# Optimization experiments

Measured on AMD Instinct MI355X. Metric: run time of the kernel, lower is better.

The kernel has to match this reference:

```python
import jax, jax.numpy as jnp
import numpy as np

DIM_Q = 512
DIM_KV = 512
HEADS = 8
EPS = 1e-5


def _layernorm(x, gamma, beta):
    mu = jnp.mean(x, axis=-1, keepdims=True)
    var = jnp.var(x, axis=-1, keepdims=True)
    return (x - mu) * jax.lax.rsqrt(var + EPS) * gamma + beta


def setup_inputs() -> dict:
    key = jax.random.key(0)
    ks = jax.random.split(key, 12)
    B, N, M = 4, 2048, 2048
    s_q = 1.0 / np.sqrt(DIM_Q)
    s_kv = 1.0 / np.sqrt(DIM_KV)
    return {
        "x": jax.random.normal(ks[0], (B, N, DIM_Q), jnp.float32),
        "context": jax.random.normal(ks[1], (B, M, DIM_KV), jnp.float32),
        "g_q": jnp.ones((DIM_Q,), jnp.float32),
        "b_q": jnp.zeros((DIM_Q,), jnp.float32),
        "g_kv": jnp.ones((DIM_KV,), jnp.float32),
        "b_kv": jnp.zeros((DIM_KV,), jnp.float32),
        "Wq": jax.random.uniform(ks[2], (DIM_Q, DIM_Q), jnp.float32, -s_q, s_q),
        "bq": jax.random.uniform(ks[3], (DIM_Q,), jnp.float32, -s_q, s_q),
        "Wk": jax.random.uniform(ks[4], (DIM_KV, DIM_Q), jnp.float32, -s_kv, s_kv),
        "bk": jax.random.uniform(ks[5], (DIM_Q,), jnp.float32, -s_kv, s_kv),
        "Wv": jax.random.uniform(ks[6], (DIM_KV, DIM_Q), jnp.float32, -s_kv, s_kv),
        "bv": jax.random.uniform(ks[7], (DIM_Q,), jnp.float32, -s_kv, s_kv),
        "Wo": jax.random.uniform(ks[8], (DIM_Q, DIM_Q), jnp.float32, -s_q, s_q),
        "bo": jax.random.uniform(ks[9], (DIM_Q,), jnp.float32, -s_q, s_q),
    }


def reference(x, context, g_q, b_q, g_kv, b_kv, Wq, bq, Wk, bk, Wv, bv, Wo, bo):
    B, N, C = x.shape
    M = context.shape[1]
    H = HEADS
    D = C // H
    scale = D ** (-0.5)

    residual = x
    xn = _layernorm(x, g_q, b_q)
    cn = _layernorm(context, g_kv, b_kv)

    # projections: [B, S, C] -> [B, H, S, D]
    q = (xn @ Wq + bq).reshape(B, N, H, D).transpose(0, 2, 1, 3)
    k = (cn @ Wk + bk).reshape(B, M, H, D).transpose(0, 2, 1, 3)
    v = (cn @ Wv + bv).reshape(B, M, H, D).transpose(0, 2, 1, 3)

    attn = jax.nn.softmax(jnp.einsum('bhnd,bhmd->bhnm', q, k) * scale, axis=-1)
    out = jnp.einsum('bhnm,bhmd->bhnd', attn, v)
    out = out.transpose(0, 2, 1, 3).reshape(B, N, C)
    # dropout is identity in eval mode
    return residual + out @ Wo + bo
```

## Files before the change

### kernel.cpp

```cpp
#include <hip/hip_runtime.h>
#include <hip/hip_bf16.h>

#define DIMC 512
#define NB   2048
#define MB   2048
#define ROWS 8192

typedef __attribute__((ext_vector_type(8))) short s8v;
typedef __attribute__((ext_vector_type(4))) short s4v;
typedef __attribute__((ext_vector_type(4))) float f4v;

__device__ __forceinline__ unsigned short cvt_bf16(float x) {
  union { float f; unsigned u; } v; v.f = x;
  unsigned r = v.u + 0x7fffu + ((v.u >> 16) & 1u);
  return (unsigned short)(r >> 16);
}

__device__ __forceinline__ void gload16(const void* g, void* l) {
  __builtin_amdgcn_global_load_lds(
      (const __attribute__((address_space(1))) unsigned int*)g,
      (__attribute__((address_space(3))) unsigned int*)l, 16, 0, 0);
}

__device__ __forceinline__ unsigned cvt_pk_bf16(float a, float b) {
  unsigned r;
  asm("v_cvt_pk_bf16_f32 %0, %1, %2" : "=v"(r) : "v"(a), "v"(b));
  return r;
}

__global__ void ln_kernel(const float* __restrict__ x, const float* __restrict__ ctx,
                          const float* __restrict__ gq, const float* __restrict__ bq,
                          const float* __restrict__ gkv, const float* __restrict__ bkv,
                          unsigned short* __restrict__ xn, unsigned short* __restrict__ cn) {
  int row  = blockIdx.x * 4 + (threadIdx.x >> 6);
  int lane = threadIdx.x & 63;
  const float* src; unsigned short* dst; const float* g; const float* b;
  if (row < ROWS) { src = x   + (size_t)row * DIMC;        dst = xn + (size_t)row * DIMC;        g = gq;  b = bq;  }
  else            { src = ctx + (size_t)(row-ROWS) * DIMC; dst = cn + (size_t)(row-ROWS) * DIMC; g = gkv; b = bkv; }

  float4 v0 = ((const float4*)src)[lane];
  float4 v1 = ((const float4*)src)[lane + 64];
  float s  = v0.x+v0.y+v0.z+v0.w + v1.x+v1.y+v1.z+v1.w;
  float ss = v0.x*v0.x+v0.y*v0.y+v0.z*v0.z+v0.w*v0.w
           + v1.x*v1.x+v1.y*v1.y+v1.z*v1.z+v1.w*v1.w;
  #pragma unroll
  for (int m = 1; m <= 32; m <<= 1) { s += __shfl_xor(s, m); ss += __shfl_xor(ss, m); }
  float mu  = s * (1.0f/512.0f);
  float var = ss * (1.0f/512.0f) - mu*mu;
  float rs  = rsqrtf(var + 1e-5f);

  int i0 = lane*4, i1 = 256 + lane*4;
  ushort4 o0, o1;
  o0.x = cvt_bf16((v0.x-mu)*rs*g[i0+0] + b[i0+0]);
  o0.y = cvt_bf16((v0.y-mu)*rs*g[i0+1] + b[i0+1]);
  o0.z = cvt_bf16((v0.z-mu)*rs*g[i0+2] + b[i0+2]);
  o0.w = cvt_bf16((v0.w-mu)*rs*g[i0+3] + b[i0+3]);
  o1.x = cvt_bf16((v1.x-mu)*rs*g[i1+0] + b[i1+0]);
  o1.y = cvt_bf16((v1.y-mu)*rs*g[i1+1] + b[i1+1]);
  o1.z = cvt_bf16((v1.z-mu)*rs*g[i1+2] + b[i1+2]);
  o1.w = cvt_bf16((v1.w-mu)*rs*g[i1+3] + b[i1+3]);
  *(ushort4*)&dst[i0] = o0;
  *(ushort4*)&dst[i1] = o1;
}

__global__ void wt_kernel(const float* __restrict__ Wq, const float* __restrict__ Wk,
                          const float* __restrict__ Wv, const float* __restrict__ Wo,
                          unsigned short* __restrict__ Wt) {
  __shared__ float tile[64][65];
  int z = blockIdx.z;
  const float* W = (z==0) ? Wq : (z==1) ? Wk : (z==2) ? Wv : Wo;
  unsigned short* dst = Wt + (size_t)z * DIMC * DIMC;
  int k0 = blockIdx.x * 64, n0 = blockIdx.y * 64;
  int tid = threadIdx.x;
  #pragma unroll
  for (int i = 0; i < 16; ++i) {
    int idx = tid + i*256; int r = idx >> 6, c = idx & 63;
    tile[r][c] = W[(size_t)(k0+r)*DIMC + n0 + c];
  }
  __syncthreads();
  #pragma unroll
  for (int i = 0; i < 16; ++i) {
    int idx = tid + i*256; int r = idx >> 6, c = idx & 63;
    dst[(size_t)(n0+r)*DIMC + k0 + c] = cvt_bf16(tile[c][r]);
  }
}

__global__ void gemm_qkv(const unsigned short* __restrict__ xn, const unsigned short* __restrict__ cnr,
                         const unsigned short* __restrict__ Wt,
                         const float* __restrict__ bq, const float* __restrict__ bk, const float* __restrict__ bv,
                         unsigned short* __restrict__ Qo, unsigned short* __restrict__ Ko,
                         unsigned short* __restrict__ Vo) {
  int z = blockIdx.z;
  const unsigned short* A = (z == 0) ? xn : cnr;
  const unsigned short* B = Wt + (size_t)z * DIMC * DIMC;
  const float* bias       = (z==0) ? bq : (z==1) ? bk : bv;
  unsigned short* C       = (z==0) ? Qo : (z==1) ? Ko : Vo;
  const float cs          = (z==0) ? 0.18033688011f : 1.0f;

  __shared__ unsigned short As[128][64];
  __shared__ unsigned short Bs[128][64];

  int tid = threadIdx.x;
  int w = tid >> 6, lane = tid & 63;
  int wr = w >> 1, wc = w & 1;
  int mBase = blockIdx.x * 128, nBase = blockIdx.y * 128;

  f4v zf = {0.f, 0.f, 0.f, 0.f};
  f4v acc[4][4];
  #pragma unroll
  for (int m = 0; m < 4; ++m)
    #pragma unroll
    for (int n = 0; n < 4; ++n) acc[m][n] = zf;

  const unsigned short* gA = A + (size_t)(mBase + (lane>>3)) * DIMC + (lane&7)*8;
  const unsigned short* gB = B + (size_t)(nBase + (lane>>3)) * DIMC + (lane&7)*8;

  for (int kt = 0; kt < 8; ++kt) {
    int k0 = kt * 64;
    if (kt) __syncthreads();
    #pragma unroll
    for (int r = 0; r < 4; ++r) {
      int row0 = r*32 + w*8;
      gload16(gA + (size_t)row0 * DIMC + k0, &As[row0][0]);
      gload16(gB + (size_t)row0 * DIMC + k0, &Bs[row0][0]);
    }
    __syncthreads();
    #pragma unroll
    for (int t = 0; t < 2; ++t) {
      s8v af[4], bfr[4];
      #pragma unroll
      for (int m = 0; m < 4; ++m)
        af[m] = *(const s8v*)&As[wr*64 + m*16 + (lane&15)][t*32 + (lane>>4)*8];
      #pragma unroll
      for (int n = 0; n < 4; ++n)
        bfr[n] = *(const s8v*)&Bs[wc*64 + n*16 + (lane&15)][t*32 + (lane>>4)*8];
      #pragma unroll
      for (int m = 0; m < 4; ++m)
        #pragma unroll
        for (int n = 0; n < 4; ++n)
          acc[m][n] = __builtin_amdgcn_mfma_f32_16x16x32_bf16(af[m], bfr[n], acc[m][n], 0, 0, 0);
    }
  }

  if (z == 2) {
    #pragma unroll
    for (int m = 0; m < 4; ++m) {
      int row = mBase + wr*64 + m*16 + (lane>>4)*4;
      int b_  = row >> 11, key = row & 2047;
      int k   = key >> 2;
      int P0  = (((k>>2)&1)<<2) + ((k&3)<<3) + ((k>>3)<<5);
      #pragma unroll
      for (int n = 0; n < 4; ++n) {
        int col = nBase + wc*64 + n*16 + (lane&15);
        float bb = bias[col];
        ushort4 st;
        st.x = cvt_bf16(acc[m][n][0] + bb);
        st.y = cvt_bf16(acc[m][n][1] + bb);
        st.z = cvt_bf16(acc[m][n][2] + bb);
        st.w = cvt_bf16(acc[m][n][3] + bb);
        *(ushort4*)&C[((size_t)(b_*8 + (col>>6))*64 + (col&63))*2048 + P0] = st;
      }
    }
  } else {
    #pragma unroll
    for (int m = 0; m < 4; ++m) {
      int row = mBase + wr*64 + m*16 + (lane>>4)*4;
      #pragma unroll
      for (int n = 0; n < 4; ++n) {
        int col = nBase + wc*64 + n*16 + (lane&15);
        float bb = bias[col];
        #pragma unroll
        for (int j = 0; j < 4; ++j)
          C[(size_t)(row+j)*DIMC + col] = cvt_bf16((acc[m][n][j] + bb) * cs);
      }
    }
  }
}

__global__ void gemm_out(const unsigned short* __restrict__ A, const unsigned short* __restrict__ Bt,
                         const float* __restrict__ bo, const float* __restrict__ resid,
                         float* __restrict__ out) {
  __shared__ unsigned short As[128][64];
  __shared__ unsigned short Bs[128][64];

  int tid = threadIdx.x;
  int w = tid >> 6, lane = tid & 63;
  int wr = w >> 1, wc = w & 1;
  int mBase = blockIdx.x * 128, nBase = blockIdx.y * 128;

  f4v zf = {0.f, 0.f, 0.f, 0.f};
  f4v acc[4][4];
  #pragma unroll
  for (int m = 0; m < 4; ++m)
    #pragma unroll
    for (int n = 0; n < 4; ++n) acc[m][n] = zf;

  const unsigned short* gA = A  + (size_t)(mBase + (lane>>3)) * DIMC + (lane&7)*8;
  const unsigned short* gB = Bt + (size_t)(nBase + (lane>>3)) * DIMC + (lane&7)*8;

  for (int kt = 0; kt < 8; ++kt) {
    int k0 = kt * 64;
    if (kt) __syncthreads();
    #pragma unroll
    for (int r = 0; r < 4; ++r) {
      int row0 = r*32 + w*8;
      gload16(gA + (size_t)row0 * DIMC + k0, &As[row0][0]);
      gload16(gB + (size_t)row0 * DIMC + k0, &Bs[row0][0]);
    }
    __syncthreads();
    #pragma unroll
    for (int t = 0; t < 2; ++t) {
      s8v af[4], bfr[4];
      #pragma unroll
      for (int m = 0; m < 4; ++m)
        af[m] = *(const s8v*)&As[wr*64 + m*16 + (lane&15)][t*32 + (lane>>4)*8];
      #pragma unroll
      for (int n = 0; n < 4; ++n)
        bfr[n] = *(const s8v*)&Bs[wc*64 + n*16 + (lane&15)][t*32 + (lane>>4)*8];
      #pragma unroll
      for (int m = 0; m < 4; ++m)
        #pragma unroll
        for (int n = 0; n < 4; ++n)
          acc[m][n] = __builtin_amdgcn_mfma_f32_16x16x32_bf16(af[m], bfr[n], acc[m][n], 0, 0, 0);
    }
  }

  #pragma unroll
  for (int m = 0; m < 4; ++m) {
    int row = mBase + wr*64 + m*16 + (lane>>4)*4;
    #pragma unroll
    for (int n = 0; n < 4; ++n) {
      int col = nBase + wc*64 + n*16 + (lane&15);
      float bb = bo[col];
      #pragma unroll
      for (int j = 0; j < 4; ++j) {
        size_t idx = (size_t)(row+j)*DIMC + col;
        out[idx] = acc[m][n][j] + bb + resid[idx];
      }
    }
  }
}

__global__ void attn_kernel(const unsigned short* __restrict__ Q, const unsigned short* __restrict__ K,
                            const unsigned short* __restrict__ Vt, unsigned short* __restrict__ O) {
  __shared__ __align__(16) char Ks[2][8192];
  __shared__ __align__(16) char Vs[2][8192];

  int tid = threadIdx.x, w = tid >> 6, lane = tid & 63;
  int slot = blockIdx.x;
  int logical = (slot & 7) * 128 + (slot >> 3);
  int qb = logical & 31;
  int bh = logical >> 5;
  int b = bh >> 3, h = bh & 7;
  size_t base  = ((size_t)b * NB) * DIMC + h * 64;
  size_t vbase = (size_t)(b*8 + h) * 64 * 2048;

  int g = lane >> 4;
  int l15 = lane & 15;

  int qrow = qb*64 + w*16 + l15;
  const s8v qf0 = *(const s8v*)&Q[base + (size_t)qrow*DIMC + g*8];
  const s8v qf1 = *(const s8v*)&Q[base + (size_t)qrow*DIMC + 32 + g*8];

  f4v zf = {0.f, 0.f, 0.f, 0.f};
  f4v o_[4];
  #pragma unroll
  for (int c = 0; c < 4; ++c) o_[c] = zf;
  f4v o5 = zf;

  s8v ones;
  #pragma unroll
  for (int e = 0; e < 8; ++e) ones[e] = (short)0x3F80;

  int sub = lane >> 3;
  int grp = ((lane & 7) ^ sub) * 8;
  const unsigned short* Kg = K + base;
  const unsigned short* Vg = Vt + vbase;
  int krow0 = w*16 + sub,  krow1 = w*16 + 8 + sub;
  unsigned sdst0 = (unsigned)(w*2048);
  unsigned sdst1 = (unsigned)(w*2048 + 1024);

  int sw = (l15 & 7) << 4;
  unsigned a0 = (unsigned)(l15*128 + ((16*g) ^ sw));
  unsigned a1 = (unsigned)(l15*128 + (((64 + 16*g)) ^ sw));

  gload16(Kg + (size_t)(krow0)*DIMC + grp, Ks[0] + sdst0);
  gload16(Kg + (size_t)(krow1)*DIMC + grp, Ks[0] + sdst1);
  gload16(Vg + (size_t)(krow0)*2048 + grp, Vs[0] + sdst0);
  gload16(Vg + (size_t)(krow1)*2048 + grp, Vs[0] + sdst1);

  #pragma unroll 1
  for (int tt = 0; tt < 16; ++tt) {
    #pragma unroll
    for (int p = 0; p < 2; ++p) {
      int t = tt*2 + p;
      const char* KsB = Ks[p];
      const char* VsB = Vs[p];
      char* KsN = Ks[p^1];
      char* VsN = Vs[p^1];

      if (t < 31) {
        int kv = (t+1)*64;
        gload16(Kg + (size_t)(kv + krow0)*DIMC + grp, KsN + sdst0);
        gload16(Kg + (size_t)(kv + krow1)*DIMC + grp, KsN + sdst1);
        gload16(Vg + (size_t)(krow0)*2048 + kv + grp, VsN + sdst0);
        gload16(Vg + (size_t)(krow1)*2048 + kv + grp, VsN + sdst1);
        asm volatile("s_waitcnt vmcnt(4)" ::: "memory");
      } else {
        asm volatile("s_waitcnt vmcnt(0)" ::: "memory");
      }
      __builtin_amdgcn_s_barrier();
      __builtin_amdgcn_sched_barrier(0);

      f4v st[4];
      #pragma unroll
      for (int c = 0; c < 4; ++c) {
        s8v ka = *(const s8v*)(KsB + c*2048 + a0);
        s8v kb = *(const s8v*)(KsB + c*2048 + a1);
        st[c] = __builtin_amdgcn_mfma_f32_16x16x32_bf16(ka, qf0, zf, 0, 0, 0);
        st[c] = __builtin_amdgcn_mfma_f32_16x16x32_bf16(kb, qf1, st[c], 0, 0, 0);
      }

      s8v vf0[4], vf1[4];
      #pragma unroll
      for (int c = 0; c < 4; ++c) {
        vf0[c] = *(const s8v*)(VsB + c*2048 + a0);
        vf1[c] = *(const s8v*)(VsB + c*2048 + a1);
      }

      float pt[4][4];
      #pragma unroll
      for (int c = 0; c < 4; ++c)
        #pragma unroll
        for (int j = 0; j < 4; ++j)
          pt[c][j] = __builtin_amdgcn_exp2f(st[c][j]);

      union { unsigned i[8]; s8v s[2]; } pu;
      pu.i[0] = cvt_pk_bf16(pt[0][0], pt[0][1]);
      pu.i[1] = cvt_pk_bf16(pt[0][2], pt[0][3]);
      pu.i[2] = cvt_pk_bf16(pt[1][0], pt[1][1]);
      pu.i[3] = cvt_pk_bf16(pt[1][2], pt[1][3]);
      pu.i[4] = cvt_pk_bf16(pt[2][0], pt[2][1]);
      pu.i[5] = cvt_pk_bf16(pt[2][2], pt[2][3]);
      pu.i[6] = cvt_pk_bf16(pt[3][0], pt[3][1]);
      pu.i[7] = cvt_pk_bf16(pt[3][2], pt[3][3]);

      #pragma unroll
      for (int c = 0; c < 4; ++c) {
        o_[c] = __builtin_amdgcn_mfma_f32_16x16x32_bf16(pu.s[0], vf0[c], o_[c], 0, 0, 0);
        o_[c] = __builtin_amdgcn_mfma_f32_16x16x32_bf16(pu.s[1], vf1[c], o_[c], 0, 0, 0);
      }
      o5 = __builtin_amdgcn_mfma_f32_16x16x32_bf16(pu.s[0], ones, o5, 0, 0, 0);
      o5 = __builtin_amdgcn_mfma_f32_16x16x32_bf16(pu.s[1], ones, o5, 0, 0, 0);

      __builtin_amdgcn_sched_barrier(0);
      __builtin_amdgcn_s_barrier();
    }
  }

  float lb[4];
  #pragma unroll
  for (int j = 0; j < 4; ++j) lb[j] = 1.0f / o5[j];
  int nrow = qb*64 + w*16 + g*4;
  #pragma unroll
  for (int c = 0; c < 4; ++c) {
    int d = h*64 + c*16 + l15;
    #pragma unroll
    for (int j = 0; j < 4; ++j)
      O[((size_t)b*NB + nrow + j) * DIMC + d] = cvt_bf16(o_[c][j] * lb[j]);
  }
}

extern "C" void kernel_launch(void* const* d_in, const int* in_sizes, int n_in,
                              void* d_out, int out_size, void* d_ws, size_t ws_size,
                              hipStream_t stream) {
  const float* x    = (const float*)d_in[0];
  const float* ctx  = (const float*)d_in[1];
  const float* g_q  = (const float*)d_in[2];
  const float* b_q  = (const float*)d_in[3];
  const float* g_kv = (const float*)d_in[4];
  const float* b_kv = (const float*)d_in[5];
  const float* Wq   = (const float*)d_in[6];
  const float* bq   = (const float*)d_in[7];
  const float* Wk   = (const float*)d_in[8];
  const float* bk   = (const float*)d_in[9];
  const float* Wv   = (const float*)d_in[10];
  const float* bv   = (const float*)d_in[11];
  const float* Wo   = (const float*)d_in[12];
  const float* bo   = (const float*)d_in[13];
  float* out = (float*)d_out;

  char* ws = (char*)d_ws;
  unsigned short* xn = (unsigned short*)(ws);
  unsigned short* cn = (unsigned short*)(ws + 8388608);
  unsigned short* Wt = (unsigned short*)(ws + 16777216);
  unsigned short* Qb = (unsigned short*)(ws + 18874368);
  unsigned short* Kb = (unsigned short*)(ws + 27262976);
  unsigned short* Vb = (unsigned short*)(ws + 35651584);
  unsigned short* Ab = cn;

  ln_kernel<<<4096, 256, 0, stream>>>(x, ctx, g_q, b_q, g_kv, b_kv, xn, cn);
  wt_kernel<<<dim3(8, 8, 4), 256, 0, stream>>>(Wq, Wk, Wv, Wo, Wt);
  gemm_qkv<<<dim3(64, 4, 3), 256, 0, stream>>>(xn, cn, Wt, bq, bk, bv, Qb, Kb, Vb);
  attn_kernel<<<1024, 256, 0, stream>>>(Qb, Kb, Vb, Ab);
  gemm_out<<<dim3(64, 4), 256, 0, stream>>>(Ab, Wt + 3*DIMC*DIMC, bo, x, out);
}
```

Before: 98.58 us.

## Split attention KV tile across wave pairs with 32-row query blocks per wave

Result: no change. 96.96 us (-1.6%).

```diff
diff --git a/kernel.cpp b/kernel.cpp
--- a/kernel.cpp
+++ b/kernel.cpp
@@ -243,10 +243,12 @@
 
 __global__ void attn_kernel(const unsigned short* __restrict__ Q, const unsigned short* __restrict__ K,
                             const unsigned short* __restrict__ Vt, unsigned short* __restrict__ O) {
-  __shared__ __align__(16) char Ks[2][8192];
-  __shared__ __align__(16) char Vs[2][8192];
+  __shared__ __align__(16) char ldsRaw[32768];
+  char* KsBuf = ldsRaw;
+  char* VsBuf = ldsRaw + 16384;
 
   int tid = threadIdx.x, w = tid >> 6, lane = tid & 63;
+  int kw = w & 1, qw = w >> 1;
   int slot = blockIdx.x;
   int logical = (slot & 7) * 128 + (slot >> 3);
   int qb = logical & 31;
@@ -258,15 +260,21 @@
   int g = lane >> 4;
   int l15 = lane & 15;
 
-  int qrow = qb*64 + w*16 + l15;
-  const s8v qf0 = *(const s8v*)&Q[base + (size_t)qrow*DIMC + g*8];
-  const s8v qf1 = *(const s8v*)&Q[base + (size_t)qrow*DIMC + 32 + g*8];
+  s8v qf[2][2];
+  #pragma unroll
+  for (int qc = 0; qc < 2; ++qc) {
+    int qrow = qb*64 + qw*32 + qc*16 + l15;
+    qf[qc][0] = *(const s8v*)&Q[base + (size_t)qrow*DIMC + g*8];
+    qf[qc][1] = *(const s8v*)&Q[base + (size_t)qrow*DIMC + 32 + g*8];
+  }
 
   f4v zf = {0.f, 0.f, 0.f, 0.f};
-  f4v o_[4];
-  #pragma unroll
-  for (int c = 0; c < 4; ++c) o_[c] = zf;
-  f4v o5 = zf;
+  f4v o_[2][4];
+  #pragma unroll
+  for (int qc = 0; qc < 2; ++qc)
+    #pragma unroll
+    for (int c = 0; c < 4; ++c) o_[qc][c] = zf;
+  f4v o5[2] = {zf, zf};
 
   s8v ones;
   #pragma unroll
@@ -274,37 +282,43 @@
 
   int sub = lane >> 3;
   int grp = ((lane & 7) ^ sub) * 8;
-  const unsigned short* Kg = K + base;
-  const unsigned short* Vg = Vt + vbase;
   int krow0 = w*16 + sub,  krow1 = w*16 + 8 + sub;
   unsigned sdst0 = (unsigned)(w*2048);
   unsigned sdst1 = (unsigned)(w*2048 + 1024);
 
+  const unsigned short* kp0 = K + base + (size_t)krow0*DIMC + grp;
+  const unsigned short* kp1 = K + base + (size_t)krow1*DIMC + grp;
+  const unsigned short* vp0 = Vt + vbase + (size_t)krow0*2048 + grp;
+  const unsigned short* vp1 = Vt + vbase + (size_t)krow1*2048 + grp;
+
   int sw = (l15 & 7) << 4;
   unsigned a0 = (unsigned)(l15*128 + ((16*g) ^ sw));
-  unsigned a1 = (unsigned)(l15*128 + (((64 + 16*g)) ^ sw));
-
-  gload16(Kg + (size_t)(krow0)*DIMC + grp, Ks[0] + sdst0);
-  gload16(Kg + (size_t)(krow1)*DIMC + grp, Ks[0] + sdst1);
-  gload16(Vg + (size_t)(krow0)*2048 + grp, Vs[0] + sdst0);
-  gload16(Vg + (size_t)(krow1)*2048 + grp, Vs[0] + sdst1);
+  unsigned a1 = (unsigned)(l15*128 + ((64 + 16*g) ^ sw));
+  unsigned av = kw ? a1 : a0;
+  unsigned kbase = (unsigned)(kw * 4096);
+
+  gload16(kp0, KsBuf + sdst0);
+  gload16(kp1, KsBuf + sdst1);
+  gload16(vp0, VsBuf + sdst0);
+  gload16(vp1, VsBuf + sdst1);
+  kp0 += 64*DIMC; kp1 += 64*DIMC; vp0 += 64; vp1 += 64;
 
   #pragma unroll 1
   for (int tt = 0; tt < 16; ++tt) {
     #pragma unroll
     for (int p = 0; p < 2; ++p) {
       int t = tt*2 + p;
-      const char* KsB = Ks[p];
-      const char* VsB = Vs[p];
-      char* KsN = Ks[p^1];
-      char* VsN = Vs[p^1];
+      const char* KsB = KsBuf + p*8192;
+      const char* VsB = VsBuf + p*8192;
+      char* KsN = KsBuf + (p^1)*8192;
+      char* VsN = VsBuf + (p^1)*8192;
 
       if (t < 31) {
-        int kv = (t+1)*64;
-        gload16(Kg + (size_t)(kv + krow0)*DIMC + grp, KsN + sdst0);
-        gload16(Kg + (size_t)(kv + krow1)*DIMC + grp, KsN + sdst1);
-        gload16(Vg + (size_t)(krow0)*2048 + kv + grp, VsN + sdst0);
-        gload16(Vg + (size_t)(krow1)*2048 + kv + grp, VsN + sdst1);
+        gload16(kp0, KsN + sdst0);
+        gload16(kp1, KsN + sdst1);
+        gload16(vp0, VsN + sdst0);
+        gload16(vp1, VsN + sdst1);
+        kp0 += 64*DIMC; kp1 += 64*DIMC; vp0 += 64; vp1 += 64;
         asm volatile("s_waitcnt vmcnt(4)" ::: "memory");
       } else {
         asm volatile("s_waitcnt vmcnt(0)" ::: "memory");
@@ -312,62 +326,86 @@
       __builtin_amdgcn_s_barrier();
       __builtin_amdgcn_sched_barrier(0);
 
-      f4v st[4];
-      #pragma unroll
-      for (int c = 0; c < 4; ++c) {
-        s8v ka = *(const s8v*)(KsB + c*2048 + a0);
-        s8v kb = *(const s8v*)(KsB + c*2048 + a1);
-        st[c] = __builtin_amdgcn_mfma_f32_16x16x32_bf16(ka, qf0, zf, 0, 0, 0);
-        st[c] = __builtin_amdgcn_mfma_f32_16x16x32_bf16(kb, qf1, st[c], 0, 0, 0);
-      }
-
-      s8v vf0[4], vf1[4];
-      #pragma unroll
-      for (int c = 0; c < 4; ++c) {
-        vf0[c] = *(const s8v*)(VsB + c*2048 + a0);
-        vf1[c] = *(const s8v*)(VsB + c*2048 + a1);
-      }
-
-      float pt[4][4];
+      s8v ka0 = *(const s8v*)(KsB + kbase        + a0);
+      s8v kh0 = *(const s8v*)(KsB + kbase        + a1);
+      s8v ka1 = *(const s8v*)(KsB + kbase + 2048 + a0);
+      s8v kh1 = *(const s8v*)(KsB + kbase + 2048 + a1);
+
+      s8v vf[4];
       #pragma unroll
       for (int c = 0; c < 4; ++c)
-        #pragma unroll
-        for (int j = 0; j < 4; ++j)
-          pt[c][j] = __builtin_amdgcn_exp2f(st[c][j]);
-
-      union { unsigned i[8]; s8v s[2]; } pu;
-      pu.i[0] = cvt_pk_bf16(pt[0][0], pt[0][1]);
-      pu.i[1] = cvt_pk_bf16(pt[0][2], pt[0][3]);
-      pu.i[2] = cvt_pk_bf16(pt[1][0], pt[1][1]);
-      pu.i[3] = cvt_pk_bf16(pt[1][2], pt[1][3]);
-      pu.i[4] = cvt_pk_bf16(pt[2][0], pt[2][1]);
-      pu.i[5] = cvt_pk_bf16(pt[2][2], pt[2][3]);
-      pu.i[6] = cvt_pk_bf16(pt[3][0], pt[3][1]);
-      pu.i[7] = cvt_pk_bf16(pt[3][2], pt[3][3]);
-
-      #pragma unroll
-      for (int c = 0; c < 4; ++c) {
-        o_[c] = __builtin_amdgcn_mfma_f32_16x16x32_bf16(pu.s[0], vf0[c], o_[c], 0, 0, 0);
-        o_[c] = __builtin_amdgcn_mfma_f32_16x16x32_bf16(pu.s[1], vf1[c], o_[c], 0, 0, 0);
-      }
-      o5 = __builtin_amdgcn_mfma_f32_16x16x32_bf16(pu.s[0], ones, o5, 0, 0, 0);
-      o5 = __builtin_amdgcn_mfma_f32_16x16x32_bf16(pu.s[1], ones, o5, 0, 0, 0);
+        vf[c] = *(const s8v*)(VsB + c*2048 + av);
+
+      f4v st[2][2];
+      #pragma unroll
+      for (int qc = 0; qc < 2; ++qc) {
+        st[qc][0] = __builtin_amdgcn_mfma_f32_16x16x32_bf16(ka0, qf[qc][0], zf, 0, 0, 0);
+        st[qc][0] = __builtin_amdgcn_mfma_f32_16x16x32_bf16(kh0, qf[qc][1], st[qc][0], 0, 0, 0);
+        st[qc][1] = __builtin_amdgcn_mfma_f32_16x16x32_bf16(ka1, qf[qc][0], zf, 0, 0, 0);
+        st[qc][1] = __builtin_amdgcn_mfma_f32_16x16x32_bf16(kh1, qf[qc][1], st[qc][1], 0, 0, 0);
+      }
+
+      #pragma unroll
+      for (int qc = 0; qc < 2; ++qc) {
+        float pt[2][4];
+        #pragma unroll
+        for (int c2 = 0; c2 < 2; ++c2)
+          #pragma unroll
+          for (int j = 0; j < 4; ++j)
+            pt[c2][j] = __builtin_amdgcn_exp2f(st[qc][c2][j]);
+
+        union { unsigned i[4]; s8v s; } pu;
+        pu.i[0] = cvt_pk_bf16(pt[0][0], pt[0][1]);
+        pu.i[1] = cvt_pk_bf16(pt[0][2], pt[0][3]);
+        pu.i[2] = cvt_pk_bf16(pt[1][0], pt[1][1]);
+        pu.i[3] = cvt_pk_bf16(pt[1][2], pt[1][3]);
+
+        #pragma unroll
+        for (int c = 0; c < 4; ++c)
+          o_[qc][c] = __builtin_amdgcn_mfma_f32_16x16x32_bf16(pu.s, vf[c], o_[qc][c], 0, 0, 0);
+        o5[qc] = __builtin_amdgcn_mfma_f32_16x16x32_bf16(pu.s, ones, o5[qc], 0, 0, 0);
+      }
 
       __builtin_amdgcn_sched_barrier(0);
       __builtin_amdgcn_s_barrier();
     }
   }
 
-  float lb[4];
-  #pragma unroll
-  for (int j = 0; j < 4; ++j) lb[j] = 1.0f / o5[j];
-  int nrow = qb*64 + w*16 + g*4;
-  #pragma unroll
-  for (int c = 0; c < 4; ++c) {
-    int d = h*64 + c*16 + l15;
-    #pragma unroll
-    for (int j = 0; j < 4; ++j)
-      O[((size_t)b*NB + nrow + j) * DIMC + d] = cvt_bf16(o_[c][j] * lb[j]);
+  float* comb = (float*)ldsRaw;
+  float* lbuf = (float*)(ldsRaw + 16640);
+
+  if (kw == 1) {
+    #pragma unroll
+    for (int qc = 0; qc < 2; ++qc) {
+      #pragma unroll
+      for (int c = 0; c < 4; ++c)
+        #pragma unroll
+        for (int j = 0; j < 4; ++j)
+          comb[(qw*32 + qc*16 + g*4 + j)*65 + c*16 + l15] = o_[qc][c][j];
+      #pragma unroll
+      for (int j = 0; j < 4; ++j)
+        lbuf[qw*32 + qc*16 + g*4 + j] = o5[qc][j];
+    }
+  }
+  __syncthreads();
+  if (kw == 0) {
+    #pragma unroll
+    for (int qc = 0; qc < 2; ++qc) {
+      float lb[4];
+      #pragma unroll
+      for (int j = 0; j < 4; ++j)
+        lb[j] = 1.0f / (o5[qc][j] + lbuf[qw*32 + qc*16 + g*4 + j]);
+      int nrow = qb*64 + qw*32 + qc*16 + g*4;
+      #pragma unroll
+      for (int c = 0; c < 4; ++c) {
+        int d = h*64 + c*16 + l15;
+        #pragma unroll
+        for (int j = 0; j < 4; ++j) {
+          float o = o_[qc][c][j] + comb[(qw*32 + qc*16 + g*4 + j)*65 + c*16 + l15];
+          O[((size_t)b*NB + nrow + j) * DIMC + d] = cvt_bf16(o * lb[j]);
+        }
+      }
+    }
   }
 }
 
```
